# Performance work log

Measured on AMD Instinct MI355X. Metric: run time of the kernel, lower is better.

The kernel has to match this reference:

```python
import jax, jax.numpy as jnp
import numpy as np

B, M, N_DIM = 2048, 1024, 64


def setup_inputs() -> dict:
    key = jax.random.key(0)
    ks = jax.random.split(key, 6)
    X = jax.random.normal(ks[0], (B, N_DIM), dtype=jnp.float32)
    Mu0 = jax.random.normal(ks[1], (M, N_DIM), dtype=jnp.float32)
    Mu1 = jax.random.normal(ks[2], (M, N_DIM), dtype=jnp.float32)
    # diagonal variances must be positive
    S0 = jax.random.uniform(ks[3], (M, N_DIM), dtype=jnp.float32, minval=0.1, maxval=1.0)
    S1 = jax.random.uniform(ks[4], (M, N_DIM), dtype=jnp.float32, minval=0.1, maxval=1.0)
    Lam = jax.random.uniform(ks[5], (M,), dtype=jnp.float32, minval=0.01, maxval=1.0)
    Lam = Lam / jnp.sum(Lam)  # transport-plan weights sum to 1
    return {"X": X, "Mu0": Mu0, "Mu1": Mu1, "S0": S0, "S1": S1,
            "Lam": Lam, "t": 0.3, "epsilon": 0.5}


def reference(X, Mu0, Mu1, S0, S1, Lam, t, epsilon):
    # GMMflow_fast.calc_u with sparse coupling of M nonzero (i,j) pairs.
    eps2 = epsilon ** 2
    Ds = jnp.sqrt(4.0 * S0 * S1 + epsilon ** 4)            # [M, n]
    Cs = 0.5 * (Ds - eps2)                                  # [M, n]
    v = Mu1 - Mu0                                           # [M, n]
    Mut = (1.0 - t) * Mu0 + t * Mu1                         # [M, n]
    Sigma = ((1.0 - t) ** 2) * S0 + (t ** 2) * S1 + 2.0 * t * (1.0 - t) * (Cs + 0.5 * eps2)
    Pt = t * S1 + (1.0 - t) * Cs
    Qt = (1.0 - t) * S0 + t * Cs
    St = Pt - Qt - eps2 * t
    K = St / Sigma                                          # [M, n]

    Xd = X[:, None, :] - Mut[None, :, :]                    # [B, M, n]
    U = K[None, :, :] * Xd + v[None, :, :]                  # [B, M, n]

    # Gaussian log-prob plus (n/2) log(2*pi), matching the torch code:
    # log N(x; mu, Sigma) + n/2 log(2pi) = -0.5 * sum(d^2/Sigma + log Sigma)
    logw = -0.5 * jnp.sum(Xd * Xd / Sigma[None, :, :] + jnp.log(Sigma)[None, :, :], axis=-1)  # [B, M]
    logw = jnp.clip(logw, -50.0, 50.0)
    W = jnp.exp(logw) * Lam[None, :]                        # [B, M]

    u = jnp.einsum('bm,bmd->bd', W, U)                      # [B, n]
    norm = jnp.sum(W, axis=1, keepdims=True)                # [B, 1]
    return u / norm
```

## Files before the change

### kernel.cpp

```cpp
#include <hip/hip_runtime.h>
#include <math.h>


#define B_N 2048
#define M_N 1024
#define NSPLIT 16
#define BT 64
#define MS 64

typedef short bf16x8 __attribute__((ext_vector_type(8)));
typedef float f32x4 __attribute__((ext_vector_type(4)));

static __device__ __forceinline__ unsigned short bf16rn(float f) {
    union { float f; unsigned u; } v; v.f = f;
    unsigned r = v.u + 0x7FFF + ((v.u >> 16) & 1);
    return (unsigned short)(r >> 16);
}
static __device__ __forceinline__ float bf2f(unsigned short h) {
    union { unsigned u; float f; } v; v.u = ((unsigned)h) << 16;
    return v.f;
}
static __device__ __forceinline__ void st4(unsigned short* p, unsigned short a,
                                           unsigned short b, unsigned short c, unsigned short d) {
    union { unsigned short u[4]; float2 f; } t;
    t.u[0] = a; t.u[1] = b; t.u[2] = c; t.u[3] = d;
    *(float2*)p = t.f;
}

__global__ __launch_bounds__(256)
void prep_kernel(const float* __restrict__ Mu0, const float* __restrict__ Mu1,
                 const float* __restrict__ S0, const float* __restrict__ S1,
                 const float* __restrict__ T, const float* __restrict__ E,
                 unsigned short* __restrict__ B1h, unsigned short* __restrict__ B1l,
                 unsigned short* __restrict__ VTh, float* __restrict__ qArr) {
    __shared__ float sK[4 * 65];
    __shared__ float sG[4 * 65];
    const int tid = threadIdx.x;
    const int m0 = blockIdx.x * 4;
    const int mi = tid >> 6, d = tid & 63;
    const int m = m0 + mi;
    const float t = T[0], e = E[0];
    const float eps2 = e * e, eps4 = eps2 * eps2, omt = 1.f - t;
    int idx = m * 64 + d;
    float s0 = S0[idx], s1 = S1[idx];
    float mu0 = Mu0[idx], mu1 = Mu1[idx];
    float Ds = sqrtf(4.f * s0 * s1 + eps4);
    float Cs = 0.5f * (Ds - eps2);
    float sig = omt * omt * s0 + t * t * s1 + 2.f * t * omt * (Cs + 0.5f * eps2);
    float St = (t * s1 + omt * Cs) - (omt * s0 + t * Cs) - eps2 * t;
    float a = 1.f / sig;
    float K = St * a;
    float mut = omt * mu0 + t * mu1;
    float pp = -2.f * mut * a;
    float g = (mu1 - mu0) - K * mut;
    unsigned short ah = bf16rn(a);
    B1h[m * 128 + d] = ah;
    B1l[m * 128 + d] = bf16rn(a - bf2f(ah));
    unsigned short ph = bf16rn(pp);
    B1h[m * 128 + 64 + d] = ph;
    B1l[m * 128 + 64 + d] = bf16rn(pp - bf2f(ph));
    sK[mi * 65 + d] = K;
    sG[mi * 65 + d] = g;
    float qd = mut * mut * a + __logf(sig);
    #pragma unroll
    for (int off = 32; off > 0; off >>= 1) qd += __shfl_xor(qd, off, 64);
    if (d == 0) qArr[m] = qd;
    __syncthreads();
    #pragma unroll
    for (int it = 0; it < 2; it++) {
        int i = it * 256 + tid;
        int n = i >> 2, mm = i & 3;
        float v = (n < 64) ? sK[mm * 65 + n] : sG[mm * 65 + (n - 64)];
        VTh[n * M_N + m0 + mm] = bf16rn(v);
    }
}

__global__ __launch_bounds__(256, 2)
void gmm_main_kernel(const float* __restrict__ X, const float* __restrict__ Lam,
                     const unsigned short* __restrict__ B1h, const unsigned short* __restrict__ B1l,
                     const unsigned short* __restrict__ VTh,
                     const float* __restrict__ qArr,
                     unsigned short* __restrict__ partBF, float* __restrict__ partN) {
    __shared__ __align__(16) char smem_raw[70144];
    unsigned short* sm = (unsigned short*)smem_raw;
    unsigned short* sA1h = sm;
    unsigned short* sA1l = sm + 8704;
    unsigned short* sB1h = sm + 17408;
    unsigned short* sB1l = sm + 26112;
    unsigned short* sV   = sm;
    unsigned short* sW   = sm + 17408;
    float* sQ = (float*)(smem_raw + 69632);
    float* sL = (float*)(smem_raw + 69888);

    const int tid  = threadIdx.x;
    const int Boff = blockIdx.x * BT;
    const int Moff = blockIdx.y * MS;
    const int w    = tid >> 6;
    const int lane = tid & 63;
    const int c = lane & 15, q = lane >> 4;
    const int wb = w >> 1;
    const int wm = w & 1;

    {
        const float4* X4 = (const float4*)X;
        #pragma unroll
        for (int it = 0; it < 4; it++) {
            int i = it * 256 + tid;
            int b = i >> 4, dq4 = i & 15;
            float4 xv = X4[(size_t)(Boff + b) * 16 + dq4];
            float xs[4] = {xv.x, xv.y, xv.z, xv.w};
            unsigned short yh[4], yl[4], xh[4], xl[4];
            #pragma unroll
            for (int k = 0; k < 4; k++) {
                float y = xs[k] * xs[k];
                yh[k] = bf16rn(y);  yl[k] = bf16rn(y - bf2f(yh[k]));
                xh[k] = bf16rn(xs[k]);  xl[k] = bf16rn(xs[k] - bf2f(xh[k]));
            }
            int base = b * 136 + 4 * dq4;
            st4(sA1h + base, yh[0], yh[1], yh[2], yh[3]);
            st4(sA1l + base, yl[0], yl[1], yl[2], yl[3]);
            st4(sA1h + base + 64, xh[0], xh[1], xh[2], xh[3]);
            st4(sA1l + base + 64, xl[0], xl[1], xl[2], xl[3]);
        }
        const float4* gBh = (const float4*)B1h + (size_t)Moff * 16;
        const float4* gBl = (const float4*)B1l + (size_t)Moff * 16;
        #pragma unroll
        for (int it = 0; it < 4; it++) {
            int i = it * 256 + tid;
            int row = i >> 4, cc = i & 15;
            *(float4*)(sB1h + row * 136 + cc * 8) = gBh[row * 16 + cc];
            *(float4*)(sB1l + row * 136 + cc * 8) = gBl[row * 16 + cc];
        }
        if (tid < 64) sQ[tid] = qArr[Moff + tid];
        else if (tid < 128) sL[tid - 64] = Lam[Moff + tid - 64];
    }
    __syncthreads();

    f32x4 acc1[2][2];
    #pragma unroll
    for (int i = 0; i < 2; i++)
        #pragma unroll
        for (int j = 0; j < 2; j++) acc1[i][j] = (f32x4){0.f, 0.f, 0.f, 0.f};
    #pragma unroll
    for (int ks = 0; ks < 4; ks++) {
        bf16x8 Ah[2], Al[2], Bh[2], Bl[2];
        #pragma unroll
        for (int i = 0; i < 2; i++) {
            int row = wb * 32 + i * 16 + c;
            Ah[i] = *(const bf16x8*)(sA1h + row * 136 + ks * 32 + q * 8);
            Al[i] = *(const bf16x8*)(sA1l + row * 136 + ks * 32 + q * 8);
        }
        #pragma unroll
        for (int j = 0; j < 2; j++) {
            int row = wm * 32 + j * 16 + c;
            Bh[j] = *(const bf16x8*)(sB1h + row * 136 + ks * 32 + q * 8);
            Bl[j] = *(const bf16x8*)(sB1l + row * 136 + ks * 32 + q * 8);
        }
        #pragma unroll
        for (int i = 0; i < 2; i++)
            #pragma unroll
            for (int j = 0; j < 2; j++) {
                acc1[i][j] = __builtin_amdgcn_mfma_f32_16x16x32_bf16(Ah[i], Bh[j], acc1[i][j], 0, 0, 0);
                acc1[i][j] = __builtin_amdgcn_mfma_f32_16x16x32_bf16(Ah[i], Bl[j], acc1[i][j], 0, 0, 0);
                acc1[i][j] = __builtin_amdgcn_mfma_f32_16x16x32_bf16(Al[i], Bh[j], acc1[i][j], 0, 0, 0);
            }
    }
    __syncthreads();

    {
        const float4* gV = (const float4*)VTh;
        int mo8 = Moff >> 3;
        #pragma unroll
        for (int it = 0; it < 4; it++) {
            int i = it * 256 + tid;
            int row = i >> 3, cc = i & 7;
            *(float4*)(sV + row * 72 + cc * 8) = gV[(size_t)row * 128 + mo8 + cc];
        }
        float nsum[2][4];
        #pragma unroll
        for (int i = 0; i < 2; i++)
            #pragma unroll
            for (int r = 0; r < 4; r++) nsum[i][r] = 0.f;
        #pragma unroll
        for (int i = 0; i < 2; i++)
            #pragma unroll
            for (int j = 0; j < 2; j++) {
                int m = wm * 32 + j * 16 + c;
                float qm = sQ[m], lm = sL[m];
                #pragma unroll
                for (int r = 0; r < 4; r++) {
                    int bl = wb * 32 + i * 16 + q * 4 + r;
                    float lw = -0.5f * (acc1[i][j][r] + qm);
                    lw = fminf(50.f, fmaxf(-50.f, lw));
                    float wf = __expf(lw) * lm;
                    unsigned short wh = bf16rn(wf);
                    sW[bl * 72 + m] = wh;
                    nsum[i][r] += bf2f(wh);
                }
            }
        #pragma unroll
        for (int mask = 1; mask <= 8; mask <<= 1)
            #pragma unroll
            for (int i = 0; i < 2; i++)
                #pragma unroll
                for (int r = 0; r < 4; r++)
                    nsum[i][r] += __shfl_xor(nsum[i][r], mask, 64);
        if (c == 0) {
            #pragma unroll
            for (int i = 0; i < 2; i++)
                #pragma unroll
                for (int r = 0; r < 4; r++) {
                    int b = Boff + wb * 32 + i * 16 + q * 4 + r;
                    partN[((size_t)blockIdx.y * B_N + b) * 2 + wm] = nsum[i][r];
                }
        }
    }
    __syncthreads();

    f32x4 acc2[2][4];
    #pragma unroll
    for (int i = 0; i < 2; i++)
        #pragma unroll
        for (int j = 0; j < 4; j++) acc2[i][j] = (f32x4){0.f, 0.f, 0.f, 0.f};
    #pragma unroll
    for (int ks = 0; ks < 2; ks++) {
        bf16x8 Wf[2], Vf[4];
        #pragma unroll
        for (int i = 0; i < 2; i++) {
            int row = wb * 32 + i * 16 + c;
            Wf[i] = *(const bf16x8*)(sW + row * 72 + ks * 32 + q * 8);
        }
        #pragma unroll
        for (int j = 0; j < 4; j++) {
            int row = wm * 64 + j * 16 + c;
            Vf[j] = *(const bf16x8*)(sV + row * 72 + ks * 32 + q * 8);
        }
        #pragma unroll
        for (int i = 0; i < 2; i++)
            #pragma unroll
            for (int j = 0; j < 4; j++)
                acc2[i][j] = __builtin_amdgcn_mfma_f32_16x16x32_bf16(Wf[i], Vf[j], acc2[i][j], 0, 0, 0);
    }

    #pragma unroll
    for (int i = 0; i < 2; i++)
        #pragma unroll
        for (int j = 0; j < 4; j++) {
            #pragma unroll
            for (int r = 0; r < 4; r++) {
                int b = Boff + wb * 32 + i * 16 + q * 4 + r;
                int n = wm * 64 + j * 16 + c;
                partBF[((size_t)blockIdx.y * B_N + b) * 128 + n] = bf16rn(acc2[i][j][r]);
            }
        }
}

__global__ __launch_bounds__(128)
void finalize_kernel(const float* __restrict__ X, const unsigned short* __restrict__ partBF,
                     const float* __restrict__ partN, float* __restrict__ out) {
    int gid = blockIdx.x * 128 + threadIdx.x;
    int b = gid >> 4, d0 = (gid & 15) * 4;
    float a1[4] = {0.f, 0.f, 0.f, 0.f}, a2[4] = {0.f, 0.f, 0.f, 0.f}, nn = 0.f;
    #pragma unroll
    for (int s = 0; s < NSPLIT; s++) {
        const unsigned short* row = partBF + ((size_t)s * B_N + b) * 128;
        ushort4 v1 = *(const ushort4*)(row + d0);
        ushort4 v2 = *(const ushort4*)(row + 64 + d0);
        a1[0] += bf2f(v1.x); a1[1] += bf2f(v1.y); a1[2] += bf2f(v1.z); a1[3] += bf2f(v1.w);
        a2[0] += bf2f(v2.x); a2[1] += bf2f(v2.y); a2[2] += bf2f(v2.z); a2[3] += bf2f(v2.w);
        float2 nv = *(const float2*)(partN + ((size_t)s * B_N + b) * 2);
        nn += nv.x + nv.y;
    }
    float rn = 1.f / nn;
    float4 xv = *(const float4*)(X + (size_t)b * 64 + d0);
    float4 o;
    o.x = (xv.x * a1[0] + a2[0]) * rn;
    o.y = (xv.y * a1[1] + a2[1]) * rn;
    o.z = (xv.z * a1[2] + a2[2]) * rn;
    o.w = (xv.w * a1[3] + a2[3]) * rn;
    *(float4*)(out + (size_t)b * 64 + d0) = o;
}

extern "C" void kernel_launch(void* const* d_in, const int* in_sizes, int n_in,
                              void* d_out, int out_size, void* d_ws, size_t ws_size,
                              hipStream_t stream) {
    (void)in_sizes; (void)n_in; (void)out_size; (void)ws_size;
    const float* X   = (const float*)d_in[0];
    const float* Mu0 = (const float*)d_in[1];
    const float* Mu1 = (const float*)d_in[2];
    const float* S0  = (const float*)d_in[3];
    const float* S1  = (const float*)d_in[4];
    const float* Lam = (const float*)d_in[5];
    const float* T   = (const float*)d_in[6];
    const float* E   = (const float*)d_in[7];

    char* ws = (char*)d_ws;
    unsigned short* B1h   = (unsigned short*)(ws);
    unsigned short* B1l   = (unsigned short*)(ws + 262144);
    unsigned short* VTh   = (unsigned short*)(ws + 524288);
    float*          qArr  = (float*)(ws + 786432);
    unsigned short* partBF= (unsigned short*)(ws + 790528);
    float*          partN = (float*)(ws + 790528 + 8388608);

    prep_kernel<<<256, 256, 0, stream>>>(Mu0, Mu1, S0, S1, T, E, B1h, B1l, VTh, qArr);
    dim3 grid(B_N / BT, NSPLIT);
    gmm_main_kernel<<<grid, 256, 0, stream>>>(X, Lam, B1h, B1l, VTh, qArr, partBF, partN);
    finalize_kernel<<<256, 128, 0, stream>>>(X, partBF, partN, (float*)d_out);
}
```

Before: 82.42 us.

## Precompute X split-bf16 operands in prep and stream tiles via direct global-to-LDS loads

X's hi/lo bf16 splitting is moved out of the main kernel, where each of the 16 M-split blocks repeated it, into extra prep blocks that write it once to workspace. The main kernel then fills shared memory for A, B and V with direct global-to-LDS loads. Shared-memory padding is replaced by an XOR swizzle that is applied when prep writes the workspace and again when fragments are read. This removes redundant conversion work and the register round-trip on tile loads. In exchange it adds workspace traffic, and the swizzle must match exactly between producer and consumer.

```diff
diff --git a/kernel.cpp b/kernel.cpp
--- a/kernel.cpp
+++ b/kernel.cpp
@@ -26,16 +26,43 @@
     t.u[0] = a; t.u[1] = b; t.u[2] = c; t.u[3] = d;
     *(float2*)p = t.f;
 }
+static __device__ __forceinline__ void gload16(const void* g, void* l) {
+    __builtin_amdgcn_global_load_lds(
+        (const __attribute__((address_space(1))) unsigned int*)g,
+        (__attribute__((address_space(3))) unsigned int*)l, 16, 0, 0);
+}
 
 __global__ __launch_bounds__(256)
-void prep_kernel(const float* __restrict__ Mu0, const float* __restrict__ Mu1,
+void prep_kernel(const float* __restrict__ X,
+                 const float* __restrict__ Mu0, const float* __restrict__ Mu1,
                  const float* __restrict__ S0, const float* __restrict__ S1,
                  const float* __restrict__ T, const float* __restrict__ E,
                  unsigned short* __restrict__ B1h, unsigned short* __restrict__ B1l,
+                 unsigned short* __restrict__ A1h, unsigned short* __restrict__ A1l,
                  unsigned short* __restrict__ VTh, float* __restrict__ qArr) {
+    const int tid = threadIdx.x;
+    if (blockIdx.x >= 256) {
+        const int b = (blockIdx.x - 256) * 16 + (tid >> 4);
+        const int d0 = (tid & 15) * 4;
+        float4 xv = ((const float4*)X)[(size_t)b * 16 + (tid & 15)];
+        float xs[4] = {xv.x, xv.y, xv.z, xv.w};
+        unsigned short yh[4], yl[4], xh[4], xl[4];
+        #pragma unroll
+        for (int k = 0; k < 4; k++) {
+            float y = xs[k] * xs[k];
+            yh[k] = bf16rn(y);     yl[k] = bf16rn(y - bf2f(yh[k]));
+            xh[k] = bf16rn(xs[k]); xl[k] = bf16rn(xs[k] - bf2f(xh[k]));
+        }
+        const int dp = d0 ^ ((b & 7) << 3);
+        const int base = b * 128;
+        st4(A1h + base + dp,      yh[0], yh[1], yh[2], yh[3]);
+        st4(A1l + base + dp,      yl[0], yl[1], yl[2], yl[3]);
+        st4(A1h + base + 64 + dp, xh[0], xh[1], xh[2], xh[3]);
+        st4(A1l + base + 64 + dp, xl[0], xl[1], xl[2], xl[3]);
+        return;
+    }
     __shared__ float sK[4 * 65];
     __shared__ float sG[4 * 65];
-    const int tid = threadIdx.x;
     const int m0 = blockIdx.x * 4;
     const int mi = tid >> 6, d = tid & 63;
     const int m = m0 + mi;
@@ -53,12 +80,13 @@
     float mut = omt * mu0 + t * mu1;
     float pp = -2.f * mut * a;
     float g = (mu1 - mu0) - K * mut;
+    const int dp = d ^ ((m & 7) << 3);
     unsigned short ah = bf16rn(a);
-    B1h[m * 128 + d] = ah;
-    B1l[m * 128 + d] = bf16rn(a - bf2f(ah));
+    B1h[m * 128 + dp] = ah;
+    B1l[m * 128 + dp] = bf16rn(a - bf2f(ah));
     unsigned short ph = bf16rn(pp);
-    B1h[m * 128 + 64 + d] = ph;
-    B1l[m * 128 + 64 + d] = bf16rn(pp - bf2f(ph));
+    B1h[m * 128 + 64 + dp] = ph;
+    B1l[m * 128 + 64 + dp] = bf16rn(pp - bf2f(ph));
     sK[mi * 65 + d] = K;
     sG[mi * 65 + d] = g;
     float qd = mut * mut * a + __logf(sig);
@@ -71,26 +99,27 @@
         int i = it * 256 + tid;
         int n = i >> 2, mm = i & 3;
         float v = (n < 64) ? sK[mm * 65 + n] : sG[mm * 65 + (n - 64)];
-        VTh[n * M_N + m0 + mm] = bf16rn(v);
+        int mg = m0 + mm;
+        VTh[n * M_N + (mg & ~63) + ((mg & 63) ^ ((n & 7) << 3))] = bf16rn(v);
     }
 }
 
 __global__ __launch_bounds__(256, 2)
-void gmm_main_kernel(const float* __restrict__ X, const float* __restrict__ Lam,
+void gmm_main_kernel(const float* __restrict__ Lam,
                      const unsigned short* __restrict__ B1h, const unsigned short* __restrict__ B1l,
+                     const unsigned short* __restrict__ A1h, const unsigned short* __restrict__ A1l,
                      const unsigned short* __restrict__ VTh,
                      const float* __restrict__ qArr,
                      unsigned short* __restrict__ partBF, float* __restrict__ partN) {
-    __shared__ __align__(16) char smem_raw[70144];
-    unsigned short* sm = (unsigned short*)smem_raw;
-    unsigned short* sA1h = sm;
-    unsigned short* sA1l = sm + 8704;
-    unsigned short* sB1h = sm + 17408;
-    unsigned short* sB1l = sm + 26112;
-    unsigned short* sV   = sm;
-    unsigned short* sW   = sm + 17408;
-    float* sQ = (float*)(smem_raw + 69632);
-    float* sL = (float*)(smem_raw + 69888);
+    __shared__ __align__(16) char smem_raw[66048];
+    const unsigned short* smA1h = (const unsigned short*)smem_raw;
+    const unsigned short* smA1l = (const unsigned short*)(smem_raw + 16384);
+    const unsigned short* smB1h = (const unsigned short*)(smem_raw + 32768);
+    const unsigned short* smB1l = (const unsigned short*)(smem_raw + 49152);
+    const unsigned short* sV = (const unsigned short*)smem_raw;
+    unsigned short* sW = (unsigned short*)(smem_raw + 16384);
+    float* sQ = (float*)(smem_raw + 65536);
+    float* sL = (float*)(smem_raw + 65792);
 
     const int tid  = threadIdx.x;
     const int Boff = blockIdx.x * BT;
@@ -100,36 +129,20 @@
     const int c = lane & 15, q = lane >> 4;
     const int wb = w >> 1;
     const int wm = w & 1;
+    const int swz = (c & 7) << 3;
 
     {
-        const float4* X4 = (const float4*)X;
-        #pragma unroll
-        for (int it = 0; it < 4; it++) {
-            int i = it * 256 + tid;
-            int b = i >> 4, dq4 = i & 15;
-            float4 xv = X4[(size_t)(Boff + b) * 16 + dq4];
-            float xs[4] = {xv.x, xv.y, xv.z, xv.w};
-            unsigned short yh[4], yl[4], xh[4], xl[4];
-            #pragma unroll
-            for (int k = 0; k < 4; k++) {
-                float y = xs[k] * xs[k];
-                yh[k] = bf16rn(y);  yl[k] = bf16rn(y - bf2f(yh[k]));
-                xh[k] = bf16rn(xs[k]);  xl[k] = bf16rn(xs[k] - bf2f(xh[k]));
-            }
-            int base = b * 136 + 4 * dq4;
-            st4(sA1h + base, yh[0], yh[1], yh[2], yh[3]);
-            st4(sA1l + base, yl[0], yl[1], yl[2], yl[3]);
-            st4(sA1h + base + 64, xh[0], xh[1], xh[2], xh[3]);
-            st4(sA1l + base + 64, xl[0], xl[1], xl[2], xl[3]);
-        }
-        const float4* gBh = (const float4*)B1h + (size_t)Moff * 16;
-        const float4* gBl = (const float4*)B1l + (size_t)Moff * 16;
-        #pragma unroll
-        for (int it = 0; it < 4; it++) {
-            int i = it * 256 + tid;
-            int row = i >> 4, cc = i & 15;
-            *(float4*)(sB1h + row * 136 + cc * 8) = gBh[row * 16 + cc];
-            *(float4*)(sB1l + row * 136 + cc * 8) = gBl[row * 16 + cc];
+        const char* gA1h = (const char*)A1h + (size_t)Boff * 256;
+        const char* gA1l = (const char*)A1l + (size_t)Boff * 256;
+        const char* gB1h = (const char*)B1h + (size_t)Moff * 256;
+        const char* gB1l = (const char*)B1l + (size_t)Moff * 256;
+        const int off = tid * 16;
+        #pragma unroll
+        for (int cc = 0; cc < 4; cc++) {
+            gload16(gA1h + cc * 4096 + off, smem_raw +         cc * 4096 + off);
+            gload16(gA1l + cc * 4096 + off, smem_raw + 16384 + cc * 4096 + off);
+            gload16(gB1h + cc * 4096 + off, smem_raw + 32768 + cc * 4096 + off);
+            gload16(gB1l + cc * 4096 + off, smem_raw + 49152 + cc * 4096 + off);
         }
         if (tid < 64) sQ[tid] = qArr[Moff + tid];
         else if (tid < 128) sL[tid - 64] = Lam[Moff + tid - 64];
@@ -143,18 +156,19 @@
         for (int j = 0; j < 2; j++) acc1[i][j] = (f32x4){0.f, 0.f, 0.f, 0.f};
     #pragma unroll
     for (int ks = 0; ks < 4; ks++) {
+        const int p = (ks * 32 + q * 8) ^ swz;
         bf16x8 Ah[2], Al[2], Bh[2], Bl[2];
         #pragma unroll
         for (int i = 0; i < 2; i++) {
             int row = wb * 32 + i * 16 + c;
-            Ah[i] = *(const bf16x8*)(sA1h + row * 136 + ks * 32 + q * 8);
-            Al[i] = *(const bf16x8*)(sA1l + row * 136 + ks * 32 + q * 8);
+            Ah[i] = *(const bf16x8*)(smA1h + row * 128 + p);
+            Al[i] = *(const bf16x8*)(smA1l + row * 128 + p);
         }
         #pragma unroll
         for (int j = 0; j < 2; j++) {
             int row = wm * 32 + j * 16 + c;
-            Bh[j] = *(const bf16x8*)(sB1h + row * 136 + ks * 32 + q * 8);
-            Bl[j] = *(const bf16x8*)(sB1l + row * 136 + ks * 32 + q * 8);
+            Bh[j] = *(const bf16x8*)(smB1h + row * 128 + p);
+            Bl[j] = *(const bf16x8*)(smB1l + row * 128 + p);
         }
         #pragma unroll
         for (int i = 0; i < 2; i++)
@@ -168,13 +182,12 @@
     __syncthreads();
 
     {
-        const float4* gV = (const float4*)VTh;
-        int mo8 = Moff >> 3;
-        #pragma unroll
-        for (int it = 0; it < 4; it++) {
-            int i = it * 256 + tid;
-            int row = i >> 3, cc = i & 7;
-            *(float4*)(sV + row * 72 + cc * 8) = gV[(size_t)row * 128 + mo8 + cc];
+        const int off = tid * 16;
+        const char* gV = (const char*)VTh;
+        #pragma unroll
+        for (int cc = 0; cc < 4; cc++) {
+            int db = cc * 4096 + off;
+            gload16(gV + (size_t)(db >> 7) * 2048 + Moff * 2 + (db & 127), smem_raw + db);
         }
         float nsum[2][4];
         #pragma unroll
@@ -194,7 +207,7 @@
                     lw = fminf(50.f, fmaxf(-50.f, lw));
                     float wf = __expf(lw) * lm;
                     unsigned short wh = bf16rn(wf);
-                    sW[bl * 72 + m] = wh;
+                    sW[bl * 64 + (m ^ ((bl & 7) << 3))] = wh;
                     nsum[i][r] += bf2f(wh);
                 }
             }
@@ -224,16 +237,17 @@
         for (int j = 0; j < 4; j++) acc2[i][j] = (f32x4){0.f, 0.f, 0.f, 0.f};
     #pragma unroll
     for (int ks = 0; ks < 2; ks++) {
+        const int p = (ks * 32 + q * 8) ^ swz;
         bf16x8 Wf[2], Vf[4];
         #pragma unroll
         for (int i = 0; i < 2; i++) {
             int row = wb * 32 + i * 16 + c;
-            Wf[i] = *(const bf16x8*)(sW + row * 72 + ks * 32 + q * 8);
+            Wf[i] = *(const bf16x8*)(sW + row * 64 + p);
         }
         #pragma unroll
         for (int j = 0; j < 4; j++) {
             int row = wm * 64 + j * 16 + c;
-            Vf[j] = *(const bf16x8*)(sV + row * 72 + ks * 32 + q * 8);
+            Vf[j] = *(const bf16x8*)(sV + row * 64 + p);
         }
         #pragma unroll
         for (int i = 0; i < 2; i++)
@@ -295,15 +309,19 @@
     const float* E   = (const float*)d_in[7];
 
     char* ws = (char*)d_ws;
-    unsigned short* B1h   = (unsigned short*)(ws);
-    unsigned short* B1l   = (unsigned short*)(ws + 262144);
-    unsigned short* VTh   = (unsigned short*)(ws + 524288);
-    float*          qArr  = (float*)(ws + 786432);
-    unsigned short* partBF= (unsigned short*)(ws + 790528);
-    float*          partN = (float*)(ws + 790528 + 8388608);
-
-    prep_kernel<<<256, 256, 0, stream>>>(Mu0, Mu1, S0, S1, T, E, B1h, B1l, VTh, qArr);
+    unsigned short* A1h   = (unsigned short*)(ws);
+    unsigned short* A1l   = (unsigned short*)(ws + 524288);
+    unsigned short* B1h   = (unsigned short*)(ws + 1048576);
+    unsigned short* B1l   = (unsigned short*)(ws + 1310720);
+    unsigned short* VTh   = (unsigned short*)(ws + 1572864);
+    float*          qArr  = (float*)(ws + 1835008);
+    unsigned short* partBF= (unsigned short*)(ws + 1839104);
+    float*          partN = (float*)(ws + 1839104 + 8388608);
+
+    prep_kernel<<<384, 256, 0, stream>>>(X, Mu0, Mu1, S0, S1, T, E,
+                                         B1h, B1l, A1h, A1l, VTh, qArr);
     dim3 grid(B_N / BT, NSPLIT);
-    gmm_main_kernel<<<grid, 256, 0, stream>>>(X, Lam, B1h, B1l, VTh, qArr, partBF, partN);
+    gmm_main_kernel<<<grid, 256, 0, stream>>>(Lam, B1h, B1l, A1h, A1l, VTh, qArr,
+                                              partBF, partN);
     finalize_kernel<<<256, 128, 0, stream>>>(X, partBF, partN, (float*)d_out);
 }
```

After: 82.50 us. No clear change (+0.1%).
